# Optimization experiments

Hardware: AMD Instinct MI355X
Metric: run time of the kernel (lower is better)

The kernel has to match this reference:

```python
import jax, jax.numpy as jnp
import numpy as np

N, H, R, E = 20000, 128, 32, 640000

def _mlp(x, W1, b1, W2, b2):
    # Linear -> SiLU -> Linear
    h = jax.nn.silu(x @ W1 + b1)
    return h @ W2 + b2

def setup_inputs() -> dict:
    key = jax.random.key(0)
    ks = jax.random.split(key, 24)
    s = 0.05
    inp = {
        "atom_node": jax.random.normal(ks[0], (N, H), jnp.float32),
        "force_node": jax.random.normal(ks[1], (N, 3, H), jnp.float32),
        "dir_edge": jax.random.normal(ks[2], (E, 3), jnp.float32),
        "dist_edge": jax.random.uniform(ks[3], (E, R), jnp.float32),
        "edge_index": jax.random.randint(ks[4], (2, E), 0, N, jnp.int64),
        # msg_mlp
        "W_msg1": jax.random.normal(ks[5], (H + R, H), jnp.float32) * s,
        "b_msg1": jnp.zeros((H,), jnp.float32),
        "W_msg2": jax.random.normal(ks[6], (H, H), jnp.float32) * s,
        "b_msg2": jnp.zeros((H,), jnp.float32),
        # vec_mlp
        "W_vec1": jax.random.normal(ks[7], (H + R, H), jnp.float32) * s,
        "b_vec1": jnp.zeros((H,), jnp.float32),
        "W_vec2": jax.random.normal(ks[8], (H, H), jnp.float32) * s,
        "b_vec2": jnp.zeros((H,), jnp.float32),
        # node_mlp
        "W_node1": jax.random.normal(ks[9], (2 * H, H), jnp.float32) * s,
        "b_node1": jnp.zeros((H,), jnp.float32),
        "W_node2": jax.random.normal(ks[10], (H, H), jnp.float32) * s,
        "b_node2": jnp.zeros((H,), jnp.float32),
        # force_mlp
        "W_force1": jax.random.normal(ks[11], (2 * H, H), jnp.float32) * s,
        "b_force1": jnp.zeros((H,), jnp.float32),
        "W_force2": jax.random.normal(ks[12], (H, H), jnp.float32) * s,
        "b_force2": jnp.zeros((H,), jnp.float32),
    }
    return inp

def reference(atom_node, force_node, dir_edge, dist_edge, edge_index,
              W_msg1, b_msg1, W_msg2, b_msg2,
              W_vec1, b_vec1, W_vec2, b_vec2,
              W_node1, b_node1, W_node2, b_node2,
              W_force1, b_force1, W_force2, b_force2):
    row, col = edge_index[0], edge_index[1]
    num_atoms = atom_node.shape[0]

    # gather source scalar features, concat with RBF distance features -> [E, H+R]
    src_feat = jnp.concatenate([atom_node[col], dist_edge], axis=-1)

    scalar_msg = _mlp(src_feat, W_msg1, b_msg1, W_msg2, b_msg2)       # [E, H]
    scalar_agg = jax.ops.segment_sum(scalar_msg, row, num_segments=num_atoms)  # [N, H]

    vec_weights = _mlp(src_feat, W_vec1, b_vec1, W_vec2, b_vec2)      # [E, H]
    vw = vec_weights[:, None, :]                                       # [E, 1, H]
    vec_msg = dir_edge[:, :, None] * vw + force_node[col] * vw         # [E, 3, H]
    vec_agg = jax.ops.segment_sum(vec_msg, row, num_segments=num_atoms)  # [N, 3, H]

    vec_invariant = jnp.sum(force_node ** 2, axis=1)                   # [N, H]
    node_input = jnp.concatenate([atom_node, scalar_agg + vec_invariant], axis=-1)
    atom_node_new = atom_node + _mlp(node_input, W_node1, b_node1, W_node2, b_node2)

    force_input = jnp.concatenate(
        [jnp.broadcast_to(atom_node[:, None, :], force_node.shape), vec_agg], axis=-1)  # [N, 3, 2H]
    force_node_new = force_node + _mlp(force_input, W_force1, b_force1, W_force2, b_force2) * force_node

    return (atom_node_new, force_node_new)
```

## Files before the change

kernel.cpp:

```cpp
#include <hip/hip_runtime.h>

#define HH 128

typedef __attribute__((ext_vector_type(8))) short bf16x8;
typedef __attribute__((ext_vector_type(4))) float f32x4;

__device__ __forceinline__ unsigned short f2bf(float f){
  unsigned int u = __builtin_bit_cast(unsigned int, f);
  u += 0x7FFFu + ((u >> 16) & 1u);
  return (unsigned short)(u >> 16);
}
__device__ __forceinline__ float bf2f(unsigned int lo16){
  return __builtin_bit_cast(float, lo16 << 16);
}
__device__ __forceinline__ float silu_f(float x){
  return x / (1.f + __expf(-x));
}
__device__ __forceinline__ bf16x8 pack8(const float* p){
  float4 u0 = *(const float4*)(p);
  float4 u1 = *(const float4*)(p + 4);
  bf16x8 t;
  t[0]=(short)f2bf(u0.x); t[1]=(short)f2bf(u0.y); t[2]=(short)f2bf(u0.z); t[3]=(short)f2bf(u0.w);
  t[4]=(short)f2bf(u1.x); t[5]=(short)f2bf(u1.y); t[6]=(short)f2bf(u1.z); t[7]=(short)f2bf(u1.w);
  return t;
}

__global__ void zero_kernel(int* __restrict__ p, int n){
  int i = blockIdx.x*256 + threadIdx.x;
  if (i < n) p[i] = 0;
}

__global__ void tobf_kernel(const float* __restrict__ in, unsigned short* __restrict__ out, int n4){
  int i = blockIdx.x*256 + threadIdx.x;
  if (i < n4){
    float4 v = *(const float4*)(in + (size_t)i*4);
    uint2 r;
    r.x = (unsigned int)f2bf(v.x) | ((unsigned int)f2bf(v.y) << 16);
    r.y = (unsigned int)f2bf(v.z) | ((unsigned int)f2bf(v.w) << 16);
    *(uint2*)(out + (size_t)i*4) = r;
  }
}

__global__ void hist_kernel(const int* __restrict__ row, int* __restrict__ deg, int E){
  int e = blockIdx.x*256 + threadIdx.x;
  if (e < E) atomicAdd(&deg[row[e]], 1);
}

__global__ void scan_kernel(const int* __restrict__ deg, int* __restrict__ rowstart,
                            int* __restrict__ cursor, int N){
  __shared__ int part[1024];
  int t = threadIdx.x;
  int chunk = (N + 1023) >> 10;
  int base = t * chunk;
  int s = 0;
  for (int j = 0; j < chunk; ++j){ int i = base + j; if (i < N) s += deg[i]; }
  part[t] = s;
  __syncthreads();
  for (int off = 1; off < 1024; off <<= 1){
    int v = (t >= off) ? part[t - off] : 0;
    __syncthreads();
    part[t] += v;
    __syncthreads();
  }
  int run = part[t] - s;
  for (int j = 0; j < chunk; ++j){
    int i = base + j;
    if (i < N){ rowstart[i] = run; cursor[i] = run; run += deg[i]; }
  }
  if (t == 1023) rowstart[N] = part[1023];
}

__global__ void scatter_kernel(const int* __restrict__ row, int* __restrict__ cursor,
                               int* __restrict__ csr, int* __restrict__ destp, int E){
  int e = blockIdx.x*256 + threadIdx.x;
  if (e < E){
    int r = row[e];
    int p = atomicAdd(&cursor[r], 1);
    csr[p] = e;
    destp[p] = r;
  }
}

__global__ __launch_bounds__(512, 2) void fused_edge_kernel(
    const unsigned short* __restrict__ atom_bf,
    const unsigned short* __restrict__ force_bf,
    const float* __restrict__ dir,  const float* __restrict__ dist,
    const int* __restrict__ colidx,
    const int* __restrict__ rowstart, const int* __restrict__ csr,
    const int* __restrict__ destp,
    const float* __restrict__ Wm1, const float* __restrict__ bm1,
    const float* __restrict__ Wm2, const float* __restrict__ bm2,
    const float* __restrict__ Wv1, const float* __restrict__ bv1,
    const float* __restrict__ Wv2, const float* __restrict__ bv2,
    float* __restrict__ scalar_agg, float* __restrict__ vec_agg,
    int N, int nchunks)
{
  __shared__ __align__(16) unsigned short sW1[128*168];
  __shared__ __align__(16) unsigned short sW2[128*136];
  __shared__ __align__(16) unsigned short hbuf[8*16*136];
  __shared__ float accU[8*3*HH];

  const int tid = threadIdx.x;
  const int w = tid >> 6, lane = tid & 63;
  const int l15 = lane & 15, lg = lane >> 4;
  unsigned short* hb = &hbuf[w*16*136];

  #pragma unroll 1
  for (int pass = 0; pass < 2; ++pass){
    const float* W1 = pass ? Wv1 : Wm1;
    const float* W2 = pass ? Wv2 : Wm2;
    const float* B1 = pass ? bv1 : bm1;
    const float* B2 = pass ? bv2 : bm2;
    __syncthreads();
    for (int idx = tid; idx < 160*128; idx += 512){
      int k = idx >> 7, c = idx & 127;
      sW1[c*168 + k] = f2bf(W1[idx]);
    }
    for (int idx = tid; idx < 128*128; idx += 512){
      int k = idx >> 7, c = idx & 127;
      sW2[c*136 + k] = f2bf(W2[idx]);
    }
    __syncthreads();
    float bb1[8], bb2[8];
    #pragma unroll
    for (int n = 0; n < 8; ++n){ bb1[n] = B1[n*16 + l15]; bb2[n] = B2[n*16 + l15]; }

    for (int chunk = blockIdx.x; chunk < nchunks; chunk += gridDim.x){
      const int i0 = chunk << 3;
      const int i1 = (i0 + 8 < N) ? (i0 + 8) : N;
      const int p0 = rowstart[i0];
      const int pend = rowstart[i1];
      {
        const int ztot = pass ? 8*3*HH : 8*HH;
        for (int idx = tid; idx < ztot; idx += 512) accU[idx] = 0.f;
      }
      __syncthreads();

      const int ntile = (pend - p0 + 127) >> 7;
      for (int t = 0; t < ntile; ++t){
        const int tb = p0 + (t << 7) + (w << 4);
        if (tb < pend){
          int pa = tb + l15;
          if (pa >= pend) pa = pend - 1;
          const int eidA = csr[pa];
          const int ca = colidx[eidA];
          bf16x8 a[5];
          {
            const unsigned short* ar = atom_bf + (size_t)ca*HH + lg*8;
            #pragma unroll
            for (int kt = 0; kt < 4; ++kt) a[kt] = *(const bf16x8*)(ar + kt*32);
            a[4] = pack8(dist + (size_t)eidA*32 + lg*8);
          }
          f32x4 acc[8];
          #pragma unroll
          for (int n = 0; n < 8; ++n){ f32x4 tt = {bb1[n],bb1[n],bb1[n],bb1[n]}; acc[n] = tt; }
          #pragma unroll
          for (int kt = 0; kt < 5; ++kt){
            #pragma unroll
            for (int n = 0; n < 8; ++n){
              bf16x8 bf = *(const bf16x8*)&sW1[(n*16 + l15)*168 + kt*32 + lg*8];
              acc[n] = __builtin_amdgcn_mfma_f32_16x16x32_bf16(a[kt], bf, acc[n], 0, 0, 0);
            }
          }
          #pragma unroll
          for (int n = 0; n < 8; ++n)
            #pragma unroll
            for (int j = 0; j < 4; ++j)
              hb[((lg<<2) + j)*136 + n*16 + l15] = f2bf(silu_f(acc[n][j]));
          f32x4 acc2[8];
          #pragma unroll
          for (int n = 0; n < 8; ++n){ f32x4 tt = {bb2[n],bb2[n],bb2[n],bb2[n]}; acc2[n] = tt; }
          #pragma unroll
          for (int kt = 0; kt < 4; ++kt){
            bf16x8 a2 = *(const bf16x8*)&hb[l15*136 + kt*32 + lg*8];
            #pragma unroll
            for (int n = 0; n < 8; ++n){
              bf16x8 bf = *(const bf16x8*)&sW2[(n*16 + l15)*136 + kt*32 + lg*8];
              acc2[n] = __builtin_amdgcn_mfma_f32_16x16x32_bf16(a2, bf, acc2[n], 0, 0, 0);
            }
          }

          if (pass == 0){
            const int pr = tb + (lg << 2);
            int dj[4];
            #pragma unroll
            for (int j = 0; j < 4; ++j){
              int p = pr + j;
              dj[j] = (p < pend) ? (destp[p] - i0) : -1;
            }
            #pragma unroll
            for (int n = 0; n < 8; ++n){
              const int h = n*16 + l15;
              int drun = -1; float vrun = 0.f;
              #pragma unroll
              for (int j = 0; j < 4; ++j){
                if (dj[j] == drun){ vrun += acc2[n][j]; }
                else {
                  if (drun >= 0) atomicAdd(&accU[drun*HH + h], vrun);
                  drun = dj[j]; vrun = acc2[n][j];
                }
              }
              if (drun >= 0) atomicAdd(&accU[drun*HH + h], vrun);
            }
          } else {
            #pragma unroll
            for (int n = 0; n < 8; ++n)
              #pragma unroll
              for (int j = 0; j < 4; ++j)
                hb[((lg<<2) + j)*136 + n*16 + l15] = f2bf(acc2[n][j]);

            const int nvalid = pend - tb;
            int myp = tb + l15;
            if (myp >= pend) myp = pend - 1;
            const int eidS = csr[myp];
            const int dstS = destp[myp] - i0;
            const int colS = colidx[eidS];
            const float dxS = dir[(size_t)eidS*3 + 0];
            const float dyS = dir[(size_t)eidS*3 + 1];
            const float dzS = dir[(size_t)eidS*3 + 2];
            const int ch = lane << 1;

            int drun = -1;
            float v00=0.f,v01=0.f,v10=0.f,v11=0.f,v20=0.f,v21=0.f;
            #pragma unroll
            for (int r = 0; r < 16; ++r){
              const int c  = __shfl(colS, r);
              const int di = __shfl(dstS, r);
              const float d0 = __shfl(dxS, r);
              const float d1 = __shfl(dyS, r);
              const float d2 = __shfl(dzS, r);
              const unsigned short* fb = force_bf + (size_t)c*3*HH + ch;
              const unsigned int f0 = *(const unsigned int*)(fb);
              const unsigned int f1 = *(const unsigned int*)(fb + HH);
              const unsigned int f2 = *(const unsigned int*)(fb + 2*HH);
              const unsigned int vw2 = *(const unsigned int*)&hb[r*136 + ch];
              const bool valid = (r < nvalid);
              const float vl = valid ? bf2f(vw2 & 0xffffu) : 0.f;
              const float vh = valid ? bf2f(vw2 >> 16) : 0.f;
              if (di != drun){
                if (drun >= 0){
                  atomicAdd(&accU[(drun*3 + 0)*HH + ch],     v00);
                  atomicAdd(&accU[(drun*3 + 0)*HH + ch + 1], v01);
                  atomicAdd(&accU[(drun*3 + 1)*HH + ch],     v10);
                  atomicAdd(&accU[(drun*3 + 1)*HH + ch + 1], v11);
                  atomicAdd(&accU[(drun*3 + 2)*HH + ch],     v20);
                  atomicAdd(&accU[(drun*3 + 2)*HH + ch + 1], v21);
                }
                drun = di;
                v00=0.f; v01=0.f; v10=0.f; v11=0.f; v20=0.f; v21=0.f;
              }
              v00 = fmaf(vl, d0 + bf2f(f0 & 0xffffu), v00);
              v01 = fmaf(vh, d0 + bf2f(f0 >> 16),     v01);
              v10 = fmaf(vl, d1 + bf2f(f1 & 0xffffu), v10);
              v11 = fmaf(vh, d1 + bf2f(f1 >> 16),     v11);
              v20 = fmaf(vl, d2 + bf2f(f2 & 0xffffu), v20);
              v21 = fmaf(vh, d2 + bf2f(f2 >> 16),     v21);
            }
            if (drun >= 0){
              atomicAdd(&accU[(drun*3 + 0)*HH + ch],     v00);
              atomicAdd(&accU[(drun*3 + 0)*HH + ch + 1], v01);
              atomicAdd(&accU[(drun*3 + 1)*HH + ch],     v10);
              atomicAdd(&accU[(drun*3 + 1)*HH + ch + 1], v11);
              atomicAdd(&accU[(drun*3 + 2)*HH + ch],     v20);
              atomicAdd(&accU[(drun*3 + 2)*HH + ch + 1], v21);
            }
          }
        }
      }
      __syncthreads();
      if (pass == 0){
        const int tot = (i1 - i0)*HH;
        for (int idx = tid; idx < tot; idx += 512)
          scalar_agg[(size_t)i0*HH + idx] = accU[idx];
      } else {
        const int tot = (i1 - i0)*3*HH;
        for (int idx = tid; idx < tot; idx += 512)
          vec_agg[(size_t)i0*3*HH + idx] = accU[idx];
      }
      __syncthreads();
    }
  }
}

template<bool IS_FORCE>
__global__ __launch_bounds__(512, 2) void node_mlp_kernel(
    const float* __restrict__ X0,
    const float* __restrict__ X1,
    const float* __restrict__ FRC,
    const float* __restrict__ W1, const float* __restrict__ b1,
    const float* __restrict__ W2, const float* __restrict__ b2,
    float* __restrict__ out, int M)
{
  __shared__ __align__(16) unsigned short sW1[128*264];
  __shared__ __align__(16) unsigned short sW2[128*136];
  __shared__ __align__(16) unsigned short hbuf[8*16*136];

  const int tid = threadIdx.x;
  for (int idx = tid; idx < 256*128; idx += 512){
    int k = idx >> 7, c = idx & 127;
    sW1[c*264 + k] = f2bf(W1[idx]);
  }
  for (int idx = tid; idx < 128*128; idx += 512){
    int k = idx >> 7, c = idx & 127;
    sW2[c*136 + k] = f2bf(W2[idx]);
  }
  __syncthreads();

  const int w = tid >> 6, lane = tid & 63;
  const int l15 = lane & 15, lg = lane >> 4;
  unsigned short* hb = &hbuf[w*16*136];

  float b1v[8], b2v[8];
  #pragma unroll
  for (int n = 0; n < 8; ++n){ b1v[n] = b1[n*16 + l15]; b2v[n] = b2[n*16 + l15]; }

  const int ntiles = (M + 127) >> 7;
  for (int tile = blockIdx.x; tile < ntiles; tile += gridDim.x){
    const int m0 = (tile << 7) + (w << 4);
    int r = m0 + l15;
    int rr = (r < M) ? r : (M - 1);

    bf16x8 a[8];
    {
      const float* x0 = X0 + (size_t)(IS_FORCE ? (rr/3) : rr) * HH + lg*8;
      #pragma unroll
      for (int kt = 0; kt < 4; ++kt) a[kt] = pack8(x0 + kt*32);
    }
    if (IS_FORCE){
      const float* x1 = X1 + (size_t)rr * HH + lg*8;
      #pragma unroll
      for (int kt = 0; kt < 4; ++kt) a[kt+4] = pack8(x1 + kt*32);
    } else {
      #pragma unroll
      for (int kt = 0; kt < 4; ++kt){
        const float* sp = X1  + (size_t)rr*HH   + kt*32 + lg*8;
        const float* fp = FRC + (size_t)rr*3*HH + kt*32 + lg*8;
        bf16x8 tv;
        #pragma unroll
        for (int q = 0; q < 8; ++q){
          float f0 = fp[q], f1 = fp[q + HH], f2 = fp[q + 2*HH];
          tv[q] = (short)f2bf(sp[q] + f0*f0 + f1*f1 + f2*f2);
        }
        a[kt+4] = tv;
      }
    }

    f32x4 acc[8];
    #pragma unroll
    for (int n = 0; n < 8; ++n){ f32x4 t = {b1v[n],b1v[n],b1v[n],b1v[n]}; acc[n] = t; }
    #pragma unroll
    for (int kt = 0; kt < 8; ++kt){
      #pragma unroll
      for (int n = 0; n < 8; ++n){
        bf16x8 bf = *(const bf16x8*)&sW1[(n*16 + l15)*264 + kt*32 + lg*8];
        acc[n] = __builtin_amdgcn_mfma_f32_16x16x32_bf16(a[kt], bf, acc[n], 0, 0, 0);
      }
    }

    #pragma unroll
    for (int n = 0; n < 8; ++n)
      #pragma unroll
      for (int j = 0; j < 4; ++j)
        hb[((lg<<2) + j)*136 + n*16 + l15] = f2bf(silu_f(acc[n][j]));

    f32x4 acc2[8];
    #pragma unroll
    for (int n = 0; n < 8; ++n){ f32x4 t = {b2v[n],b2v[n],b2v[n],b2v[n]}; acc2[n] = t; }
    #pragma unroll
    for (int kt = 0; kt < 4; ++kt){
      bf16x8 a2 = *(const bf16x8*)&hb[l15*136 + kt*32 + lg*8];
      #pragma unroll
      for (int n = 0; n < 8; ++n){
        bf16x8 bf = *(const bf16x8*)&sW2[(n*16 + l15)*136 + kt*32 + lg*8];
        acc2[n] = __builtin_amdgcn_mfma_f32_16x16x32_bf16(a2, bf, acc2[n], 0, 0, 0);
      }
    }

    #pragma unroll
    for (int n = 0; n < 8; ++n){
      #pragma unroll
      for (int j = 0; j < 4; ++j){
        int R = m0 + (lg<<2) + j;
        if (R < M){
          size_t o = (size_t)R*HH + n*16 + l15;
          float y = acc2[n][j];
          float res;
          if (IS_FORCE){ float f = FRC[o]; res = f + y*f; }
          else         { res = X0[o] + y; }
          out[o] = res;
        }
      }
    }
  }
}

extern "C" void kernel_launch(void* const* d_in, const int* in_sizes, int n_in,
                              void* d_out, int out_size, void* d_ws, size_t ws_size,
                              hipStream_t stream)
{
  const float* atom  = (const float*)d_in[0];
  const float* force = (const float*)d_in[1];
  const float* dir   = (const float*)d_in[2];
  const float* dist  = (const float*)d_in[3];
  const int*   eidx  = (const int*)d_in[4];
  const float* Wm1 = (const float*)d_in[5];  const float* bm1 = (const float*)d_in[6];
  const float* Wm2 = (const float*)d_in[7];  const float* bm2 = (const float*)d_in[8];
  const float* Wv1 = (const float*)d_in[9];  const float* bv1 = (const float*)d_in[10];
  const float* Wv2 = (const float*)d_in[11]; const float* bv2 = (const float*)d_in[12];
  const float* Wn1 = (const float*)d_in[13]; const float* bn1 = (const float*)d_in[14];
  const float* Wn2 = (const float*)d_in[15]; const float* bn2 = (const float*)d_in[16];
  const float* Wf1 = (const float*)d_in[17]; const float* bf1 = (const float*)d_in[18];
  const float* Wf2 = (const float*)d_in[19]; const float* bf2 = (const float*)d_in[20];

  const int N = in_sizes[0] / HH;
  const int E = in_sizes[2] / 3;
  const int* rowi = eidx;
  const int* coli = eidx + E;

  char* ws = (char*)d_ws;
  size_t off = 0;
  auto take = [&](size_t bytes) -> void* {
    void* p = (void*)(ws + off);
    off += (bytes + 255) & ~(size_t)255;
    return p;
  };
  int* deg      = (int*)take((size_t)(N+1)*4);
  int* rowstart = (int*)take((size_t)(N+1)*4);
  int* cursor   = (int*)take((size_t)N*4);
  int* csr      = (int*)take((size_t)E*4);
  int* destp    = (int*)take((size_t)E*4);
  unsigned short* atom_bf  = (unsigned short*)take((size_t)N*HH*2);
  unsigned short* force_bf = (unsigned short*)take((size_t)N*3*HH*2);
  if (off > ws_size) return;
  (void)n_in; (void)out_size;

  float* out0 = (float*)d_out;
  float* out1 = out0 + (size_t)N*HH;

  zero_kernel<<<(N+256)/256, 256, 0, stream>>>(deg, N+1);
  hist_kernel<<<(E+255)/256, 256, 0, stream>>>(rowi, deg, E);
  scan_kernel<<<1, 1024, 0, stream>>>(deg, rowstart, cursor, N);
  scatter_kernel<<<(E+255)/256, 256, 0, stream>>>(rowi, cursor, csr, destp, E);

  const int na4 = N*HH/4, nf4 = N*3*HH/4;
  tobf_kernel<<<(na4+255)/256, 256, 0, stream>>>(atom,  atom_bf,  na4);
  tobf_kernel<<<(nf4+255)/256, 256, 0, stream>>>(force, force_bf, nf4);

  const int nchunks = (N + 7) >> 3;
  int fgrid = nchunks < 256 ? nchunks : 256;
  fused_edge_kernel<<<fgrid, 512, 0, stream>>>(atom_bf, force_bf, dir, dist, coli,
      rowstart, csr, destp,
      Wm1,bm1,Wm2,bm2, Wv1,bv1,Wv2,bv2,
      out0, out1, N, nchunks);

  int nt_node  = (N + 127) >> 7;
  int nt_force = (3*N + 127) >> 7;
  node_mlp_kernel<false><<<nt_node, 512, 0, stream>>>(atom, out0, force,
      Wn1,bn1,Wn2,bn2, out0, N);
  node_mlp_kernel<true><<<nt_force, 512, 0, stream>>>(atom, out1, force,
      Wf1,bf1,Wf2,bf2, out1, 3*N);
}
```

Baseline: 846.9 us.

## Pretranspose weights to bf16 once and read MFMA B operands from global memory

Adds a small kernel that converts each MLP weight matrix to transposed bf16 once per call, removing the per-block fp32 load, convert and LDS staging in the edge and node kernels. The MFMA B operands are now read straight from global memory and L2 instead of shared memory. With the large LDS weight buffers gone, the edge kernel's grid is raised from 256 to 768 blocks to use the extra occupancy. The trade-off is that every weight fragment read in the inner loops now goes through the vector memory path rather than LDS, and eight extra small kernel launches are added.

```diff
diff --git a/kernel.cpp b/kernel.cpp
--- a/kernel.cpp
+++ b/kernel.cpp
@@ -38,6 +38,14 @@
     r.x = (unsigned int)f2bf(v.x) | ((unsigned int)f2bf(v.y) << 16);
     r.y = (unsigned int)f2bf(v.z) | ((unsigned int)f2bf(v.w) << 16);
     *(uint2*)(out + (size_t)i*4) = r;
+  }
+}
+
+__global__ void wtr_kernel(const float* __restrict__ W, unsigned short* __restrict__ wT, int K){
+  int idx = blockIdx.x*256 + threadIdx.x;
+  if (idx < K*128){
+    int k = idx >> 7, c = idx & 127;
+    wT[c*K + k] = f2bf(W[idx]);
   }
 }
 
@@ -88,15 +96,13 @@
     const int* __restrict__ colidx,
     const int* __restrict__ rowstart, const int* __restrict__ csr,
     const int* __restrict__ destp,
-    const float* __restrict__ Wm1, const float* __restrict__ bm1,
-    const float* __restrict__ Wm2, const float* __restrict__ bm2,
-    const float* __restrict__ Wv1, const float* __restrict__ bv1,
-    const float* __restrict__ Wv2, const float* __restrict__ bv2,
+    const unsigned short* __restrict__ mT1, const float* __restrict__ bm1,
+    const unsigned short* __restrict__ mT2, const float* __restrict__ bm2,
+    const unsigned short* __restrict__ vT1, const float* __restrict__ bv1,
+    const unsigned short* __restrict__ vT2, const float* __restrict__ bv2,
     float* __restrict__ scalar_agg, float* __restrict__ vec_agg,
     int N, int nchunks)
 {
-  __shared__ __align__(16) unsigned short sW1[128*168];
-  __shared__ __align__(16) unsigned short sW2[128*136];
   __shared__ __align__(16) unsigned short hbuf[8*16*136];
   __shared__ float accU[8*3*HH];
 
@@ -107,19 +113,10 @@
 
   #pragma unroll 1
   for (int pass = 0; pass < 2; ++pass){
-    const float* W1 = pass ? Wv1 : Wm1;
-    const float* W2 = pass ? Wv2 : Wm2;
+    const unsigned short* T1 = pass ? vT1 : mT1;
+    const unsigned short* T2 = pass ? vT2 : mT2;
     const float* B1 = pass ? bv1 : bm1;
     const float* B2 = pass ? bv2 : bm2;
-    __syncthreads();
-    for (int idx = tid; idx < 160*128; idx += 512){
-      int k = idx >> 7, c = idx & 127;
-      sW1[c*168 + k] = f2bf(W1[idx]);
-    }
-    for (int idx = tid; idx < 128*128; idx += 512){
-      int k = idx >> 7, c = idx & 127;
-      sW2[c*136 + k] = f2bf(W2[idx]);
-    }
     __syncthreads();
     float bb1[8], bb2[8];
     #pragma unroll
@@ -158,7 +155,7 @@
           for (int kt = 0; kt < 5; ++kt){
             #pragma unroll
             for (int n = 0; n < 8; ++n){
-              bf16x8 bf = *(const bf16x8*)&sW1[(n*16 + l15)*168 + kt*32 + lg*8];
+              bf16x8 bf = *(const bf16x8*)(T1 + (n*16 + l15)*160 + kt*32 + lg*8);
               acc[n] = __builtin_amdgcn_mfma_f32_16x16x32_bf16(a[kt], bf, acc[n], 0, 0, 0);
             }
           }
@@ -175,7 +172,7 @@
             bf16x8 a2 = *(const bf16x8*)&hb[l15*136 + kt*32 + lg*8];
             #pragma unroll
             for (int n = 0; n < 8; ++n){
-              bf16x8 bf = *(const bf16x8*)&sW2[(n*16 + l15)*136 + kt*32 + lg*8];
+              bf16x8 bf = *(const bf16x8*)(T2 + (n*16 + l15)*128 + kt*32 + lg*8);
               acc2[n] = __builtin_amdgcn_mfma_f32_16x16x32_bf16(a2, bf, acc2[n], 0, 0, 0);
             }
           }
@@ -287,25 +284,13 @@
     const float* __restrict__ X0,
     const float* __restrict__ X1,
     const float* __restrict__ FRC,
-    const float* __restrict__ W1, const float* __restrict__ b1,
-    const float* __restrict__ W2, const float* __restrict__ b2,
+    const unsigned short* __restrict__ wT1, const float* __restrict__ b1,
+    const unsigned short* __restrict__ wT2, const float* __restrict__ b2,
     float* __restrict__ out, int M)
 {
-  __shared__ __align__(16) unsigned short sW1[128*264];
-  __shared__ __align__(16) unsigned short sW2[128*136];
   __shared__ __align__(16) unsigned short hbuf[8*16*136];
 
   const int tid = threadIdx.x;
-  for (int idx = tid; idx < 256*128; idx += 512){
-    int k = idx >> 7, c = idx & 127;
-    sW1[c*264 + k] = f2bf(W1[idx]);
-  }
-  for (int idx = tid; idx < 128*128; idx += 512){
-    int k = idx >> 7, c = idx & 127;
-    sW2[c*136 + k] = f2bf(W2[idx]);
-  }
-  __syncthreads();
-
   const int w = tid >> 6, lane = tid & 63;
   const int l15 = lane & 15, lg = lane >> 4;
   unsigned short* hb = &hbuf[w*16*136];
@@ -352,7 +337,7 @@
     for (int kt = 0; kt < 8; ++kt){
       #pragma unroll
       for (int n = 0; n < 8; ++n){
-        bf16x8 bf = *(const bf16x8*)&sW1[(n*16 + l15)*264 + kt*32 + lg*8];
+        bf16x8 bf = *(const bf16x8*)(wT1 + (n*16 + l15)*256 + kt*32 + lg*8);
         acc[n] = __builtin_amdgcn_mfma_f32_16x16x32_bf16(a[kt], bf, acc[n], 0, 0, 0);
       }
     }
@@ -371,7 +356,7 @@
       bf16x8 a2 = *(const bf16x8*)&hb[l15*136 + kt*32 + lg*8];
       #pragma unroll
       for (int n = 0; n < 8; ++n){
-        bf16x8 bf = *(const bf16x8*)&sW2[(n*16 + l15)*136 + kt*32 + lg*8];
+        bf16x8 bf = *(const bf16x8*)(wT2 + (n*16 + l15)*128 + kt*32 + lg*8);
         acc2[n] = __builtin_amdgcn_mfma_f32_16x16x32_bf16(a2, bf, acc2[n], 0, 0, 0);
       }
     }
@@ -431,6 +416,14 @@
   int* destp    = (int*)take((size_t)E*4);
   unsigned short* atom_bf  = (unsigned short*)take((size_t)N*HH*2);
   unsigned short* force_bf = (unsigned short*)take((size_t)N*3*HH*2);
+  unsigned short* mT1 = (unsigned short*)take(160*128*2);
+  unsigned short* mT2 = (unsigned short*)take(128*128*2);
+  unsigned short* vT1 = (unsigned short*)take(160*128*2);
+  unsigned short* vT2 = (unsigned short*)take(128*128*2);
+  unsigned short* nT1 = (unsigned short*)take(256*128*2);
+  unsigned short* nT2 = (unsigned short*)take(128*128*2);
+  unsigned short* fT1 = (unsigned short*)take(256*128*2);
+  unsigned short* fT2 = (unsigned short*)take(128*128*2);
   if (off > ws_size) return;
   (void)n_in; (void)out_size;
 
@@ -446,17 +439,26 @@
   tobf_kernel<<<(na4+255)/256, 256, 0, stream>>>(atom,  atom_bf,  na4);
   tobf_kernel<<<(nf4+255)/256, 256, 0, stream>>>(force, force_bf, nf4);
 
+  wtr_kernel<<<(160*128+255)/256, 256, 0, stream>>>(Wm1, mT1, 160);
+  wtr_kernel<<<(128*128+255)/256, 256, 0, stream>>>(Wm2, mT2, 128);
+  wtr_kernel<<<(160*128+255)/256, 256, 0, stream>>>(Wv1, vT1, 160);
+  wtr_kernel<<<(128*128+255)/256, 256, 0, stream>>>(Wv2, vT2, 128);
+  wtr_kernel<<<(256*128+255)/256, 256, 0, stream>>>(Wn1, nT1, 256);
+  wtr_kernel<<<(128*128+255)/256, 256, 0, stream>>>(Wn2, nT2, 128);
+  wtr_kernel<<<(256*128+255)/256, 256, 0, stream>>>(Wf1, fT1, 256);
+  wtr_kernel<<<(128*128+255)/256, 256, 0, stream>>>(Wf2, fT2, 128);
+
   const int nchunks = (N + 7) >> 3;
-  int fgrid = nchunks < 256 ? nchunks : 256;
+  int fgrid = nchunks < 768 ? nchunks : 768;
   fused_edge_kernel<<<fgrid, 512, 0, stream>>>(atom_bf, force_bf, dir, dist, coli,
       rowstart, csr, destp,
-      Wm1,bm1,Wm2,bm2, Wv1,bv1,Wv2,bv2,
+      mT1,bm1, mT2,bm2, vT1,bv1, vT2,bv2,
       out0, out1, N, nchunks);
 
   int nt_node  = (N + 127) >> 7;
   int nt_force = (3*N + 127) >> 7;
   node_mlp_kernel<false><<<nt_node, 512, 0, stream>>>(atom, out0, force,
-      Wn1,bn1,Wn2,bn2, out0, N);
+      nT1,bn1, nT2,bn2, out0, N);
   node_mlp_kernel<true><<<nt_force, 512, 0, stream>>>(atom, out1, force,
-      Wf1,bf1,Wf2,bf2, out1, 3*N);
-}
+      fT1,bf1, fT2,bf2, out1, 3*N);
+}
```

Measured after the change: 1.341 ms. +58.3%, slower.
